# Performance work log

Measured on AMD Instinct MI355X. Metric: run time of the kernel, lower is better.

The kernel has to match this reference:

```python
import jax, jax.numpy as jnp
import numpy as np
from jax import lax

B, S, L, H, D_IN, W = 128, 64, 137, 128, 64, 256  # batch, segments, logsig_dim, hidden, input_dim, vf_width


def setup_inputs() -> dict:
    key = jax.random.key(0)
    ks = jax.random.split(key, 12)
    rn = lambda k, s, sc: jax.random.normal(k, s, dtype=jnp.float32) * sc
    return {
        "times": jnp.arange(S + 1, dtype=jnp.float32),
        "logsig": rn(ks[0], (B, S, L), 0.1),
        "initial": rn(ks[1], (B, D_IN), 1.0),
        "in_w": rn(ks[2], (D_IN, H), 0.12),
        "in_b": rn(ks[3], (H,), 0.05),
        "h1_w": rn(ks[4], (H, W), 0.09),
        "h1_b": rn(ks[5], (W,), 0.05),
        "h2_w": rn(ks[6], (W, W), 0.06),
        "h2_b": rn(ks[7], (W,), 0.05),
        "vo_w": rn(ks[8], (W, W), 0.06),
        "vo_b": rn(ks[9], (W,), 0.05),
        "ml_w": rn(ks[10], (W, H * (L - 1)), 0.02),
        "ml_b": rn(ks[11], (H * (L - 1),), 0.01),
    }


def reference(times, logsig, initial, in_w, in_b, h1_w, h1_b, h2_w, h2_b, vo_w, vo_b, ml_w, ml_b):
    intervals = times                 # [S+1]; forward requires times == registered intervals
    coeffs = logsig[:, :, 1:]         # [B, S, L-1] (first logsig channel dropped)
    h0 = initial @ in_w + in_b        # [B, H]

    def func(t, y):
        # searchsorted + clamp, exactly as in the torch module
        idx = jnp.clip(jnp.searchsorted(intervals, t, side='left'), 1, S)
        dt = intervals[idx] - intervals[idx - 1]
        coeff = jnp.take(coeffs, idx - 1, axis=1)        # [B, L-1]
        h = jax.nn.relu(y @ h1_w + h1_b)                 # vf MLP (vf_depth-1 = 2 hidden layers)
        h = jax.nn.relu(h @ h2_w + h2_b)
        h = jnp.tanh(h @ vo_w + vo_b)                    # final tanh activation
        vf = (h @ ml_w + ml_b).reshape(B, H, L - 1)      # [B, H, L-1]
        return jnp.einsum('bhd,bd->bh', vf, coeff) / dt  # [B, H]

    def step(y, n):
        # one fixed-size Heun (RK2) step from intervals[n] to intervals[n+1]
        t0, t1 = intervals[n], intervals[n + 1]
        dt = t1 - t0
        k1 = func(t0, y)
        k2 = func(t1, y + dt * k1)
        y1 = y + 0.5 * dt * (k1 + k2)
        return y1, y1

    _, ys = lax.scan(step, h0, jnp.arange(S))            # ys: [S, B, H]
    features = jnp.concatenate([h0[:, None, :], jnp.swapaxes(ys, 0, 1)], axis=1)  # [B, S+1, H]
    return features, features[:, -1]
```

## Files before the change

### kernel.cpp

```cpp
#include <hip/hip_runtime.h>
#include <hip/hip_bf16.h>


#define BB 128
#define SS 64
#define LL 137
#define HH 128
#define DIN 64
#define WW 256
#define DD 136
#define KP 160
#define NC 32768
#define OUT2_OFF ((size_t)BB*(SS+1)*HH)

typedef __hip_bfloat16 bf16;
typedef __attribute__((ext_vector_type(8))) short short8;
typedef __attribute__((ext_vector_type(4))) float f32x4;
typedef _Float16 h2t __attribute__((ext_vector_type(2)));

__device__ __forceinline__ bf16 f2bf(float x){ return __float2bfloat16(x); }

__device__ __forceinline__ float fdot2u(unsigned w, unsigned y, float acc){
#if __has_builtin(__builtin_amdgcn_fdot2)
  return __builtin_amdgcn_fdot2(__builtin_bit_cast(h2t, w),
                                __builtin_bit_cast(h2t, y), acc, false);
#else
  h2t a = __builtin_bit_cast(h2t, w), b2 = __builtin_bit_cast(h2t, y);
  return acc + (float)a[0]*(float)b2[0] + (float)a[1]*(float)b2[1];
#endif
}
__device__ __forceinline__ float dot8(uint4 w, uint4 y, float acc){
  acc = fdot2u(w.x, y.x, acc);
  acc = fdot2u(w.y, y.y, acc);
  acc = fdot2u(w.z, y.z, acc);
  acc = fdot2u(w.w, y.w, acc);
  return acc;
}

__device__ __forceinline__ float fast_tanh(float x){
  float e = __expf(2.f*x);
#if __has_builtin(__builtin_amdgcn_rcpf)
  float r = __builtin_amdgcn_rcpf(e + 1.f);
#else
  float r = 1.f/(e + 1.f);
#endif
  return 1.f - 2.f*r;
}

__global__ void prep_coeff(const float* __restrict__ logsig, bf16* __restrict__ cA){
  int m = blockIdx.x;
  int d = threadIdx.x;
  int a = m >> 7, b = m & 127;
  float v = 0.0f;
  if (d < DD) v = logsig[(size_t)(b*SS + a)*LL + 1 + d];
  cA[(size_t)m*KP + d] = f2bf(v);
}

__global__ void prep_btt(const float* __restrict__ mlw, bf16* __restrict__ btt){
  int c = blockIdx.x;
  int d = threadIdx.x;
  int w = ((c >> 10) << 3) | (c & 7);
  int h = (c >> 3) & 127;
  float v = 0.0f;
  if (d < DD) v = mlw[(size_t)w*(HH*DD) + h*DD + d];
  btt[(size_t)c*KP + d] = f2bf(v);
}

__global__ void prep_packw(const float* __restrict__ src, uint4* __restrict__ dst){
  int c = blockIdx.x, j = threadIdx.x;
  union { _Float16 h[8]; uint4 v; } u;
  #pragma unroll
  for (int r = 0; r < 8; ++r) u.h[r] = (_Float16)src[(size_t)(c*8+r)*WW + j];
  dst[c*WW + j] = u.v;
}

__global__ void abias_kernel(const float* __restrict__ mlb, const float* __restrict__ logsig,
                             float* __restrict__ Abias){
  int a = blockIdx.x, b = blockIdx.y;
  int h = threadIdx.x;
  __shared__ float cf[DD];
  for (int d = h; d < DD; d += HH) cf[d] = logsig[(size_t)(b*SS + a)*LL + 1 + d];
  __syncthreads();
  float acc = 0.f;
  const float* mb = mlb + (size_t)h*DD;
  #pragma unroll 8
  for (int d = 0; d < DD; ++d) acc += cf[d] * mb[d];
  Abias[((size_t)a*BB + b)*HH + h] = acc;
}

#define AST 40
#define ASM_SZ (5*64*AST)
#define BSM_SZ (5*128*AST)
__global__ __launch_bounds__(256, 2) void agemm_kernel(const bf16* __restrict__ cA,
                                                       const bf16* __restrict__ btt,
                                                       _Float16* __restrict__ As, int mAbs0){
  __shared__ __align__(16) short sm[ASM_SZ + BSM_SZ];
  short* a_sm = sm;
  short* b_sm = sm + ASM_SZ;
  int mt = blockIdx.x, nt = blockIdx.y;
  int t = threadIdx.x, lane = t & 63, wid = t >> 6;
  int mBlockAbs = mAbs0 + mt*64;
  int c0 = nt*128;
  int mW = (wid & 1)*32, cW = (wid >> 1)*64;

  #pragma unroll
  for (int r = 0; r < 5; ++r){
    int idx = t + r*256;
    int kk = idx >> 8, rem = idx & 255;
    int row = rem >> 2, seg = rem & 3;
    uint4 v = *(const uint4*)(cA + (size_t)(mBlockAbs+row)*KP + kk*32 + seg*8);
    *(uint4*)&a_sm[(kk*64 + row)*AST + seg*8] = v;
  }
  #pragma unroll
  for (int r = 0; r < 10; ++r){
    int idx = t + r*256;
    int kk = idx >> 9, rem = idx & 511;
    int row = rem >> 2, seg = rem & 3;
    uint4 v = *(const uint4*)(btt + (size_t)(c0+row)*KP + kk*32 + seg*8);
    *(uint4*)&b_sm[(kk*128 + row)*AST + seg*8] = v;
  }
  __syncthreads();

  f32x4 acc[2][4];
  #pragma unroll
  for (int i = 0; i < 2; ++i)
    #pragma unroll
    for (int j = 0; j < 4; ++j)
      acc[i][j] = (f32x4){0.f,0.f,0.f,0.f};

  int mr = lane & 15, q = lane >> 4;
  #pragma unroll
  for (int kk = 0; kk < 5; ++kk){
    short8 af[2], bfr[4];
    #pragma unroll
    for (int mi = 0; mi < 2; ++mi)
      af[mi]  = *(const short8*)&a_sm[(kk*64 + mW + mi*16 + mr)*AST + q*8];
    #pragma unroll
    for (int ci = 0; ci < 4; ++ci)
      bfr[ci] = *(const short8*)&b_sm[(kk*128 + cW + ci*16 + mr)*AST + q*8];
    #pragma unroll
    for (int mi = 0; mi < 2; ++mi)
      #pragma unroll
      for (int ci = 0; ci < 4; ++ci)
        acc[mi][ci] = __builtin_amdgcn_mfma_f32_16x16x32_bf16(af[mi], bfr[ci], acc[mi][ci], 0, 0, 0);
  }
  __syncthreads();

  #pragma unroll
  for (int mi = 0; mi < 2; ++mi)
    #pragma unroll
    for (int ci = 0; ci < 4; ++ci){
      int col = cW + ci*16 + mr;
      #pragma unroll
      for (int r = 0; r < 4; ++r){
        int row = mW + mi*16 + q*4 + r;
        _Float16 hv = (_Float16)acc[mi][ci][r];
        sm[row*136 + col] = *(short*)&hv;
      }
    }
  __syncthreads();
  int mLocBlock = mt*64;
  #pragma unroll
  for (int rep = 0; rep < 4; ++rep){
    int idx = t + rep*256;
    int row = idx >> 4, seg = idx & 15;
    uint4 v = *(const uint4*)&sm[row*136 + seg*8];
    *(uint4*)(As + (size_t)(mLocBlock + row)*NC + c0 + seg*8) = v;
  }
}

__device__ __forceinline__ void nrde_func(
    int b, int wave, int lane,
    const uint4* __restrict__ wp1, const uint4* __restrict__ wp2,
    const uint4* vo_sm,
    const _Float16* yh, _Float16* h1h, _Float16* h2h, _Float16* h3h,
    const float* bs1, const float* bs2, const float* bsv,
    const _Float16* __restrict__ As, const float* __restrict__ Abias,
    int aLoc, int aAbs, float inv_dtf, float* kout)
{
  const int j  = (wave << 4) | (lane & 15);
  const int q  = lane >> 4;
  const int h  = (wave << 3) | (lane & 7);
  const int q8 = lane >> 3;

  uint4 w1r[4], w2r[8], ar[4];
  {
    const uint4* wp = wp1 + (q << 2)*WW + j;
    #pragma unroll
    for (int cc = 0; cc < 4; ++cc) w1r[cc] = wp[cc*WW];
  }
  {
    const uint4* wp = wp2 + (q << 3)*WW + j;
    #pragma unroll
    for (int cc = 0; cc < 8; ++cc) w2r[cc] = wp[cc*WW];
  }
  {
    const uint4* Ap = (const uint4*)(As + ((size_t)aLoc*BB + b)*NC);
    #pragma unroll
    for (int cc = 0; cc < 4; ++cc) ar[cc] = Ap[((q8 << 2) + cc)*HH + h];
  }
  float ab = (q8 == 0) ? Abias[((size_t)aAbs*BB + b)*HH + h] : 0.f;

  {
    const uint4* yp = (const uint4*)yh + (q << 2);
    float a0 = 0.f, a1 = 0.f;
    a0 = dot8(w1r[0], yp[0], a0); a1 = dot8(w1r[1], yp[1], a1);
    a0 = dot8(w1r[2], yp[2], a0); a1 = dot8(w1r[3], yp[3], a1);
    float acc = a0 + a1;
    acc += __shfl_xor(acc, 16);
    acc += __shfl_xor(acc, 32);
    if (q == 0){ float v = bs1[j] + acc; h1h[j] = (_Float16)(v > 0.f ? v : 0.f); }
  }
  __syncthreads();
  {
    const uint4* hp = (const uint4*)h1h + (q << 3);
    float a0 = 0.f, a1 = 0.f;
    #pragma unroll
    for (int cc = 0; cc < 8; cc += 2){
      a0 = dot8(w2r[cc],   hp[cc],   a0);
      a1 = dot8(w2r[cc+1], hp[cc+1], a1);
    }
    float acc = a0 + a1;
    acc += __shfl_xor(acc, 16);
    acc += __shfl_xor(acc, 32);
    if (q == 0){ float v = bs2[j] + acc; h2h[j] = (_Float16)(v > 0.f ? v : 0.f); }
  }
  __syncthreads();
  {
    const uint4* wp = vo_sm + (q << 3)*WW + j;
    const uint4* hp = (const uint4*)h2h + (q << 3);
    float a0 = 0.f, a1 = 0.f;
    #pragma unroll
    for (int cc = 0; cc < 8; cc += 2){
      a0 = dot8(wp[cc*WW],     hp[cc],   a0);
      a1 = dot8(wp[(cc+1)*WW], hp[cc+1], a1);
    }
    float acc = a0 + a1;
    acc += __shfl_xor(acc, 16);
    acc += __shfl_xor(acc, 32);
    if (q == 0) h3h[j] = (_Float16)fast_tanh(bsv[j] + acc);
  }
  __syncthreads();
  {
    const uint4* hp = (const uint4*)h3h + (q8 << 2);
    float a0 = 0.f, a1 = 0.f;
    a0 = dot8(ar[0], hp[0], a0); a1 = dot8(ar[1], hp[1], a1);
    a0 = dot8(ar[2], hp[2], a0); a1 = dot8(ar[3], hp[3], a1);
    float acc = a0 + a1 + ab;
    acc += __shfl_xor(acc, 8);
    acc += __shfl_xor(acc, 16);
    acc += __shfl_xor(acc, 32);
    if (q8 == 0) kout[h] = acc * inv_dtf;
  }
}

__global__ __launch_bounds__(1024) void scan_kernel(
    const float* __restrict__ times, const float* __restrict__ initial,
    const float* __restrict__ in_w, const float* __restrict__ in_b,
    const float* __restrict__ h1_b, const float* __restrict__ h2_b,
    const float* __restrict__ vo_b,
    const uint4* __restrict__ wp1, const uint4* __restrict__ wp2,
    const uint4* __restrict__ wpv,
    const _Float16* __restrict__ As, const float* __restrict__ Abias,
    float* __restrict__ y_state, float* __restrict__ out,
    int s0, int s1, int aBase)
{
  __shared__ __align__(16) uint4 vo_sm[32*WW];
  __shared__ __align__(16) _Float16 yh[HH];
  __shared__ __align__(16) _Float16 h1h[WW];
  __shared__ __align__(16) _Float16 h2h[WW];
  __shared__ __align__(16) _Float16 h3h[WW];
  __shared__ float yv[HH], kk1[HH], kk2[HH];
  __shared__ float bs1[WW], bs2[WW], bsv[WW];

  const int b = blockIdx.x, t = threadIdx.x;
  const int wave = t >> 6, lane = t & 63;

  for (int i = t; i < 32*WW; i += 1024) vo_sm[i] = wpv[i];
  if (t < WW){ bs1[t] = h1_b[t]; bs2[t] = h2_b[t]; bsv[t] = vo_b[t]; }

  if (s0 == 0){
    if (t < HH){
      float acc = in_b[t];
      for (int i = 0; i < DIN; ++i)
        acc += initial[b*DIN + i] * in_w[(size_t)i*HH + t];
      yv[t] = acc; yh[t] = (_Float16)acc;
      out[(size_t)b*(SS+1)*HH + t] = acc;
    }
  } else if (t < HH){
    float v = y_state[b*HH + t];
    yv[t] = v; yh[t] = (_Float16)v;
  }
  __syncthreads();

  for (int n = s0; n < s1; ++n){
    float t0v = times[n], t1v = times[n+1];
    float dt = t1v - t0v;
    int idx1 = (n >= 1) ? n : 1;
    float dtf1 = times[idx1] - times[idx1-1];
    int a1 = (n >= 1) ? (n-1) : 0;
    nrde_func(b, wave, lane, wp1, wp2, vo_sm, yh, h1h, h2h, h3h, bs1, bs2, bsv,
              As, Abias, a1 - aBase, a1, 1.f/dtf1, kk1);
    __syncthreads();
    if (t < HH) yh[t] = (_Float16)(yv[t] + dt*kk1[t]);
    __syncthreads();
    nrde_func(b, wave, lane, wp1, wp2, vo_sm, yh, h1h, h2h, h3h, bs1, bs2, bsv,
              As, Abias, n - aBase, n, 1.f/dt, kk2);
    __syncthreads();
    if (t < HH){
      float ynew = yv[t] + 0.5f*dt*(kk1[t] + kk2[t]);
      yv[t] = ynew; yh[t] = (_Float16)ynew;
      out[((size_t)b*(SS+1) + (n+1))*HH + t] = ynew;
    }
    __syncthreads();
  }

  if (t < HH){
    y_state[b*HH + t] = yv[t];
    if (s1 == SS) out[OUT2_OFF + (size_t)b*HH + t] = yv[t];
  }
}

extern "C" void kernel_launch(void* const* d_in, const int* in_sizes, int n_in,
                              void* d_out, int out_size, void* d_ws, size_t ws_size,
                              hipStream_t stream)
{
  (void)in_sizes; (void)n_in; (void)out_size;
  const float* times   = (const float*)d_in[0];
  const float* logsig  = (const float*)d_in[1];
  const float* initial = (const float*)d_in[2];
  const float* in_w    = (const float*)d_in[3];
  const float* in_b    = (const float*)d_in[4];
  const float* h1_w    = (const float*)d_in[5];
  const float* h1_b    = (const float*)d_in[6];
  const float* h2_w    = (const float*)d_in[7];
  const float* h2_b    = (const float*)d_in[8];
  const float* vo_w    = (const float*)d_in[9];
  const float* vo_b    = (const float*)d_in[10];
  const float* ml_w    = (const float*)d_in[11];
  const float* ml_b    = (const float*)d_in[12];
  float* out = (float*)d_out;

  char* ws = (char*)d_ws;
  size_t off = 0;
  bf16* cA      = (bf16*)(ws + off); off += (size_t)8192*KP*2;
  bf16* btt     = (bf16*)(ws + off); off += (size_t)NC*KP*2;
  float* Abias  = (float*)(ws + off); off += (size_t)SS*BB*HH*4;
  float* y_state= (float*)(ws + off); off += (size_t)BB*HH*4;
  uint4* wp1    = (uint4*)(ws + off); off += (size_t)16*WW*16;
  uint4* wp2    = (uint4*)(ws + off); off += (size_t)32*WW*16;
  uint4* wpv    = (uint4*)(ws + off); off += (size_t)32*WW*16;
  _Float16* As  = (_Float16*)(ws + off);
  size_t perA = (size_t)BB*HH*WW*2;
  size_t avail = (ws_size > off) ? (ws_size - off) : 0;
  int C = (int)(avail / perA);
  if (C > SS) C = SS;
  if (C < 2) return;

  prep_coeff<<<8192, 160, 0, stream>>>(logsig, cA);
  prep_btt<<<NC, 160, 0, stream>>>(ml_w, btt);
  abias_kernel<<<dim3(SS, BB), HH, 0, stream>>>(ml_b, logsig, Abias);
  prep_packw<<<16, WW, 0, stream>>>(h1_w, wp1);
  prep_packw<<<32, WW, 0, stream>>>(h2_w, wp2);
  prep_packw<<<32, WW, 0, stream>>>(vo_w, wpv);

  int s = 0, aB = 0;
  while (s < SS){
    int cc = SS - aB; if (cc > C) cc = C;
    agemm_kernel<<<dim3(cc*2, 256), 256, 0, stream>>>(cA, btt, As, aB*BB);
    int sEnd = aB + cc; if (sEnd > SS) sEnd = SS;
    scan_kernel<<<BB, 1024, 0, stream>>>(times, initial, in_w, in_b,
        h1_b, h2_b, vo_b, wp1, wp2, wpv, As, Abias, y_state, out, s, sEnd, aB);
    s = sEnd;
    aB = sEnd - 1;
  }
}
```

Before: 695.5 us.

## Enlarge agemm tiles with double-buffered K loads and fuse Heun updates in scan

The A-matrix GEMM now uses 128x256 tiles with 512 threads. K-slices are double-buffered in shared memory so the next global load overlaps the current MFMAs, and the f16 writeback layout uses an XOR swizzle to reduce bank conflicts. In the scan kernel, nrde_func returns k directly in registers, and the Heun stage updates are applied by the reducing lanes. This removes the kk1/kk2 shared arrays and two block-wide barriers per step. The trade-off is higher register pressure from the larger accumulator tile and a sync inside every K iteration.

Result: slower. 724.5 us (+4.2%).

```diff
diff --git a/kernel.cpp b/kernel.cpp
--- a/kernel.cpp
+++ b/kernel.cpp
@@ -89,94 +89,102 @@
 }
 
 #define AST 40
-#define ASM_SZ (5*64*AST)
-#define BSM_SZ (5*128*AST)
-__global__ __launch_bounds__(256, 2) void agemm_kernel(const bf16* __restrict__ cA,
-                                                       const bf16* __restrict__ btt,
-                                                       _Float16* __restrict__ As, int mAbs0){
-  __shared__ __align__(16) short sm[ASM_SZ + BSM_SZ];
-  short* a_sm = sm;
-  short* b_sm = sm + ASM_SZ;
+__global__ __launch_bounds__(512) void agemm_kernel(const bf16* __restrict__ cA,
+                                                    const bf16* __restrict__ btt,
+                                                    _Float16* __restrict__ As, int mAbs0){
+  __shared__ __align__(16) short sm[32768];
   int mt = blockIdx.x, nt = blockIdx.y;
   int t = threadIdx.x, lane = t & 63, wid = t >> 6;
-  int mBlockAbs = mAbs0 + mt*64;
-  int c0 = nt*128;
-  int mW = (wid & 1)*32, cW = (wid >> 1)*64;
-
-  #pragma unroll
-  for (int r = 0; r < 5; ++r){
-    int idx = t + r*256;
-    int kk = idx >> 8, rem = idx & 255;
-    int row = rem >> 2, seg = rem & 3;
-    uint4 v = *(const uint4*)(cA + (size_t)(mBlockAbs+row)*KP + kk*32 + seg*8);
-    *(uint4*)&a_sm[(kk*64 + row)*AST + seg*8] = v;
-  }
-  #pragma unroll
-  for (int r = 0; r < 10; ++r){
-    int idx = t + r*256;
-    int kk = idx >> 9, rem = idx & 511;
-    int row = rem >> 2, seg = rem & 3;
-    uint4 v = *(const uint4*)(btt + (size_t)(c0+row)*KP + kk*32 + seg*8);
-    *(uint4*)&b_sm[(kk*128 + row)*AST + seg*8] = v;
-  }
-  __syncthreads();
-
-  f32x4 acc[2][4];
-  #pragma unroll
-  for (int i = 0; i < 2; ++i)
+  int mBlockAbs = mAbs0 + mt*128;
+  int c0 = nt*256;
+  int mW = (wid & 1)*64, cW = (wid >> 1)*64;
+  const int mr = lane & 15, q = lane >> 4;
+  const int srow = t >> 2, sseg = t & 3;
+
+  {
+    uint4 va  = *(const uint4*)(cA  + (size_t)(mBlockAbs + srow)*KP + sseg*8);
+    uint4 vb0 = *(const uint4*)(btt + (size_t)(c0 + srow)*KP + sseg*8);
+    uint4 vb1 = *(const uint4*)(btt + (size_t)(c0 + 128 + srow)*KP + sseg*8);
+    *(uint4*)&sm[0     + srow*AST + sseg*8] = va;
+    *(uint4*)&sm[10240 + srow*AST + sseg*8] = vb0;
+    *(uint4*)&sm[10240 + (128 + srow)*AST + sseg*8] = vb1;
+  }
+  __syncthreads();
+
+  f32x4 acc[4][4];
+  #pragma unroll
+  for (int i = 0; i < 4; ++i)
     #pragma unroll
     for (int j = 0; j < 4; ++j)
       acc[i][j] = (f32x4){0.f,0.f,0.f,0.f};
 
-  int mr = lane & 15, q = lane >> 4;
   #pragma unroll
   for (int kk = 0; kk < 5; ++kk){
-    short8 af[2], bfr[4];
-    #pragma unroll
-    for (int mi = 0; mi < 2; ++mi)
-      af[mi]  = *(const short8*)&a_sm[(kk*64 + mW + mi*16 + mr)*AST + q*8];
+    const int cur = kk & 1;
+    const int aBase = cur ? 5120 : 0;
+    const int bBase = cur ? 20480 : 10240;
+    uint4 va, vb0, vb1;
+    if (kk < 4){
+      int d0 = (kk+1)*32;
+      va  = *(const uint4*)(cA  + (size_t)(mBlockAbs + srow)*KP + d0 + sseg*8);
+      vb0 = *(const uint4*)(btt + (size_t)(c0 + srow)*KP + d0 + sseg*8);
+      vb1 = *(const uint4*)(btt + (size_t)(c0 + 128 + srow)*KP + d0 + sseg*8);
+    }
+    short8 af[4], bfr[4];
+    #pragma unroll
+    for (int mi = 0; mi < 4; ++mi)
+      af[mi]  = *(const short8*)&sm[aBase + (mW + mi*16 + mr)*AST + q*8];
     #pragma unroll
     for (int ci = 0; ci < 4; ++ci)
-      bfr[ci] = *(const short8*)&b_sm[(kk*128 + cW + ci*16 + mr)*AST + q*8];
-    #pragma unroll
-    for (int mi = 0; mi < 2; ++mi)
+      bfr[ci] = *(const short8*)&sm[bBase + (cW + ci*16 + mr)*AST + q*8];
+    #pragma unroll
+    for (int mi = 0; mi < 4; ++mi)
       #pragma unroll
       for (int ci = 0; ci < 4; ++ci)
         acc[mi][ci] = __builtin_amdgcn_mfma_f32_16x16x32_bf16(af[mi], bfr[ci], acc[mi][ci], 0, 0, 0);
-  }
-  __syncthreads();
-
-  #pragma unroll
-  for (int mi = 0; mi < 2; ++mi)
+    if (kk < 4){
+      const int aN = cur ? 0 : 5120;
+      const int bN = cur ? 10240 : 20480;
+      *(uint4*)&sm[aN + srow*AST + sseg*8] = va;
+      *(uint4*)&sm[bN + srow*AST + sseg*8] = vb0;
+      *(uint4*)&sm[bN + (128 + srow)*AST + sseg*8] = vb1;
+    }
+    __syncthreads();
+  }
+
+  #pragma unroll
+  for (int mi = 0; mi < 4; ++mi)
     #pragma unroll
     for (int ci = 0; ci < 4; ++ci){
       int col = cW + ci*16 + mr;
       #pragma unroll
       for (int r = 0; r < 4; ++r){
         int row = mW + mi*16 + q*4 + r;
+        int cs = col ^ (((row >> 2) & 3) << 3);
         _Float16 hv = (_Float16)acc[mi][ci][r];
-        sm[row*136 + col] = *(short*)&hv;
+        sm[row*256 + cs] = *(short*)&hv;
       }
     }
   __syncthreads();
-  int mLocBlock = mt*64;
-  #pragma unroll
-  for (int rep = 0; rep < 4; ++rep){
-    int idx = t + rep*256;
-    int row = idx >> 4, seg = idx & 15;
-    uint4 v = *(const uint4*)&sm[row*136 + seg*8];
+  int mLocBlock = mt*128;
+  #pragma unroll
+  for (int rep = 0; rep < 8; ++rep){
+    int idx = t + rep*512;
+    int row = idx >> 5, seg = idx & 31;
+    int cs = (seg*8) ^ (((row >> 2) & 3) << 3);
+    uint4 v = *(const uint4*)&sm[row*256 + cs];
     *(uint4*)(As + (size_t)(mLocBlock + row)*NC + c0 + seg*8) = v;
   }
 }
 
-__device__ __forceinline__ void nrde_func(
+__device__ __forceinline__ float nrde_func(
     int b, int wave, int lane,
     const uint4* __restrict__ wp1, const uint4* __restrict__ wp2,
     const uint4* vo_sm,
     const _Float16* yh, _Float16* h1h, _Float16* h2h, _Float16* h3h,
     const float* bs1, const float* bs2, const float* bsv,
     const _Float16* __restrict__ As, const float* __restrict__ Abias,
-    int aLoc, int aAbs, float inv_dtf, float* kout)
+    int aLoc, int aAbs, float inv_dtf)
 {
   const int j  = (wave << 4) | (lane & 15);
   const int q  = lane >> 4;
@@ -199,7 +207,7 @@
     #pragma unroll
     for (int cc = 0; cc < 4; ++cc) ar[cc] = Ap[((q8 << 2) + cc)*HH + h];
   }
-  float ab = (q8 == 0) ? Abias[((size_t)aAbs*BB + b)*HH + h] : 0.f;
+  float ab = Abias[((size_t)aAbs*BB + b)*HH + h];
 
   {
     const uint4* yp = (const uint4*)yh + (q << 2);
@@ -246,11 +254,11 @@
     float a0 = 0.f, a1 = 0.f;
     a0 = dot8(ar[0], hp[0], a0); a1 = dot8(ar[1], hp[1], a1);
     a0 = dot8(ar[2], hp[2], a0); a1 = dot8(ar[3], hp[3], a1);
-    float acc = a0 + a1 + ab;
+    float acc = a0 + a1;
     acc += __shfl_xor(acc, 8);
     acc += __shfl_xor(acc, 16);
     acc += __shfl_xor(acc, 32);
-    if (q8 == 0) kout[h] = acc * inv_dtf;
+    return (acc + ab) * inv_dtf;
   }
 }
 
@@ -270,11 +278,13 @@
   __shared__ __align__(16) _Float16 h1h[WW];
   __shared__ __align__(16) _Float16 h2h[WW];
   __shared__ __align__(16) _Float16 h3h[WW];
-  __shared__ float yv[HH], kk1[HH], kk2[HH];
+  __shared__ float yv[HH];
   __shared__ float bs1[WW], bs2[WW], bsv[WW];
 
   const int b = blockIdx.x, t = threadIdx.x;
   const int wave = t >> 6, lane = t & 63;
+  const int h = (wave << 3) | (lane & 7);
+  const bool tail = (lane >> 3) == 0;
 
   for (int i = t; i < 32*WW; i += 1024) vo_sm[i] = wpv[i];
   if (t < WW){ bs1[t] = h1_b[t]; bs2[t] = h2_b[t]; bsv[t] = vo_b[t]; }
@@ -299,25 +309,23 @@
     int idx1 = (n >= 1) ? n : 1;
     float dtf1 = times[idx1] - times[idx1-1];
     int a1 = (n >= 1) ? (n-1) : 0;
-    nrde_func(b, wave, lane, wp1, wp2, vo_sm, yh, h1h, h2h, h3h, bs1, bs2, bsv,
-              As, Abias, a1 - aBase, a1, 1.f/dtf1, kk1);
+    float k1 = nrde_func(b, wave, lane, wp1, wp2, vo_sm, yh, h1h, h2h, h3h,
+                         bs1, bs2, bsv, As, Abias, a1 - aBase, a1, 1.f/dtf1);
+    if (tail) yh[h] = (_Float16)(yv[h] + dt*k1);
     __syncthreads();
-    if (t < HH) yh[t] = (_Float16)(yv[t] + dt*kk1[t]);
+    float k2 = nrde_func(b, wave, lane, wp1, wp2, vo_sm, yh, h1h, h2h, h3h,
+                         bs1, bs2, bsv, As, Abias, n - aBase, n, 1.f/dt);
+    if (tail){
+      float ynew = yv[h] + 0.5f*dt*(k1 + k2);
+      yv[h] = ynew; yh[h] = (_Float16)ynew;
+      out[((size_t)b*(SS+1) + (n+1))*HH + h] = ynew;
+    }
     __syncthreads();
-    nrde_func(b, wave, lane, wp1, wp2, vo_sm, yh, h1h, h2h, h3h, bs1, bs2, bsv,
-              As, Abias, n - aBase, n, 1.f/dt, kk2);
-    __syncthreads();
-    if (t < HH){
-      float ynew = yv[t] + 0.5f*dt*(kk1[t] + kk2[t]);
-      yv[t] = ynew; yh[t] = (_Float16)ynew;
-      out[((size_t)b*(SS+1) + (n+1))*HH + t] = ynew;
-    }
-    __syncthreads();
-  }
-
-  if (t < HH){
-    y_state[b*HH + t] = yv[t];
-    if (s1 == SS) out[OUT2_OFF + (size_t)b*HH + t] = yv[t];
+  }
+
+  if (tail){
+    y_state[b*HH + h] = yv[h];
+    if (s1 == SS) out[OUT2_OFF + (size_t)b*HH + h] = yv[h];
   }
 }
 
@@ -367,7 +375,7 @@
   int s = 0, aB = 0;
   while (s < SS){
     int cc = SS - aB; if (cc > C) cc = C;
-    agemm_kernel<<<dim3(cc*2, 256), 256, 0, stream>>>(cA, btt, As, aB*BB);
+    agemm_kernel<<<dim3(cc, 128), 512, 0, stream>>>(cA, btt, As, aB*BB);
     int sEnd = aB + cc; if (sEnd > SS) sEnd = SS;
     scan_kernel<<<BB, 1024, 0, stream>>>(times, initial, in_w, in_b,
         h1_b, h2_b, vo_b, wp1, wp2, wpv, As, Abias, y_state, out, s, sEnd, aB);
```
